# Optimization experiments

Hardware: AMD Instinct MI355X
Metric: run time of the kernel (lower is better)

## Reference

```python
import jax, jax.numpy as jnp
import numpy as np

BINS = 50
MIN_V = 0.0
MAX_V = 1.0
SIGMA = 10.0
DELTA = (MAX_V - MIN_V) / BINS
EPS = 1e-8


def _soft_bin(v, centers):
    # v: [N, D] -> [N, bins, D]
    d = v[:, None, :] - centers[None, :, None]
    return jax.nn.sigmoid(SIGMA * (d + DELTA / 2)) - jax.nn.sigmoid(SIGMA * (d - DELTA / 2))


def setup_inputs() -> dict:
    key = jax.random.key(0)
    k1, k2 = jax.random.split(key)
    im1 = jax.random.uniform(k1, (8, 384, 384), dtype=jnp.float32)
    im2 = jax.random.uniform(k2, (8, 384, 384), dtype=jnp.float32)
    return {"im1": im1, "im2": im2}


def reference(im1, im2):
    n = im1.shape[0]
    x = im1.reshape(n, -1)
    y = im2.reshape(n, -1)
    centers = MIN_V + DELTA * (jnp.arange(BINS, dtype=jnp.float32) + 0.5)
    xs = _soft_bin(x, centers)  # [N, bins, D]
    ys = _soft_bin(y, centers)  # [N, bins, D]
    hgram = jnp.einsum('nbd,ncd->nbc', xs, ys)  # [N, bins, bins]
    # NOTE: original normalizes by the sum over the WHOLE batch
    p_xy = hgram / jnp.sum(hgram)
    marginal_x = jnp.sum(p_xy, axis=2)  # [N, bins]
    marginal_y = jnp.sum(p_xy, axis=1)  # [N, bins]
    joined = marginal_x[:, :, None] * marginal_y[:, None, :]  # [N, bins, bins]
    mi_per = jnp.sum(
        p_xy * (jnp.log(p_xy + EPS) - jnp.log(joined + EPS)), axis=(1, 2)
    )
    return jnp.sum(mi_per)  # reduction='sum'
```

## Files before the change

### kernel.cpp

```cpp
#include <hip/hip_runtime.h>


#define D_TOTAL   147456
#define NBATCH    8
#define BINS      50
#define NEDGE     28
#define KSLICES   96
#define KC        256
#define SLICE_LEN (D_TOTAL / KSLICES)
#define ITERS     (SLICE_LEN / KC)
#define LDS_STR   280

typedef _Float16 half8  __attribute__((ext_vector_type(8)));
typedef __fp16   fp16x2 __attribute__((ext_vector_type(2)));
typedef float    f32x4  __attribute__((ext_vector_type(4)));

struct Tab { float c[NEDGE]; };
constexpr Tab make_tab() {
    Tab t{};
    double c = 0.6703200460356393;
    const double lam = 1.4918246976412703;
    for (int i = 0; i < NEDGE; ++i) { t.c[i] = (float)c; c *= lam; }
    return t;
}
constexpr Tab TAB = make_tab();

__global__ __launch_bounds__(256, 3) void hgram_kernel(const float* __restrict__ im1,
                                                       const float* __restrict__ im2,
                                                       float* __restrict__ hg) {
    __shared__ __align__(16) _Float16 Xs[32][LDS_STR];
    __shared__ __align__(16) _Float16 Ys[32][LDS_STR];

    const int tid   = threadIdx.x;
    const int slice = blockIdx.x;
    const int n     = blockIdx.y;
    const int base  = n * D_TOTAL + slice * SLICE_LEN;

    {
        unsigned* px = (unsigned*)&Xs[28][0];
        unsigned* py = (unsigned*)&Ys[28][0];
        for (int i = tid; i < 4 * LDS_STR / 2; i += 256) { px[i] = 0u; py[i] = 0u; }
    }

    const int h    = tid & 127;
    const int isY  = tid >> 7;
    const float2* src2 = (const float2*)((isY ? im2 : im1) + base);
    _Float16* plane = isY ? &Ys[0][0] : &Xs[0][0];
    _Float16* dst   = plane + 2 * h;

    const int lane = tid & 63;
    const int w    = tid >> 6;
    const int r0   = (w & 1) << 4;
    const int c0   = (w >> 1) << 4;
    const int frow = lane & 15;
    const int kg   = (lane >> 4) << 3;

    f32x4 acc = {0.f, 0.f, 0.f, 0.f};

    float2 v = src2[h];
    for (int it = 0; it < ITERS; ++it) {
        float2 nv = {0.f, 0.f};
        if (it + 1 < ITERS) nv = src2[(it + 1) * (KC / 2) + h];
        {
            const float Ea = __builtin_amdgcn_exp2f(v.x * -14.426950408889634f);
            const float Eb = __builtin_amdgcn_exp2f(v.y * -14.426950408889634f);
            #pragma unroll
            for (int i = 0; i < NEDGE; ++i) {
                const float c = TAB.c[i];
                float ta = __builtin_amdgcn_rcpf(__builtin_fmaf(c * Ea, 0.00390625f, 0.00390625f));
                float tb = __builtin_amdgcn_rcpf(__builtin_fmaf(c * Eb, 0.00390625f, 0.00390625f));
                fp16x2 p = __builtin_amdgcn_cvt_pkrtz(ta, tb);
                *(fp16x2*)(dst + i * LDS_STR) = p;
            }
        }
        __syncthreads();
        #pragma unroll
        for (int ks = 0; ks < 8; ++ks) {
            const int k0 = ks * 32 + kg;
            half8 a = *(const half8*)&Xs[r0 + frow][k0];
            half8 b = *(const half8*)&Ys[c0 + frow][k0];
            acc = __builtin_amdgcn_mfma_f32_16x16x32_f16(a, b, acc, 0, 0, 0);
        }
        __syncthreads();
        v = nv;
    }

    float* hgn = hg + n * 1024;
    const int gj = c0 + (lane & 15);
    const int ri = r0 + ((lane >> 4) << 2);
    if (gj < NEDGE) {
        #pragma unroll
        for (int r = 0; r < 4; ++r) {
            const int gi = ri + r;
            if (gi < NEDGE) atomicAdd(&hgn[gi * 32 + gj], acc[r]);
        }
    }
}

__global__ __launch_bounds__(1024) void finalize_kernel(const float* __restrict__ hg,
                                                        float* __restrict__ out) {
    __shared__ float Gs[NBATCH][NEDGE][29];
    __shared__ float mx[NBATCH][BINS], my[NBATCH][BINS];
    __shared__ float red[16];
    __shared__ float sT;
    const int tid = threadIdx.x;

    for (int idx = tid; idx < NBATCH * NEDGE * NEDGE; idx += 1024) {
        int n = idx / (NEDGE * NEDGE);
        int rem = idx - n * (NEDGE * NEDGE);
        int r = rem / NEDGE, c = rem - r * NEDGE;
        Gs[n][r][c] = hg[n * 1024 + r * 32 + c];
    }
    __syncthreads();

    if (tid < 2 * NBATCH * BINS) {
        const int which = (tid >= NBATCH * BINS) ? 1 : 0;
        const int t2 = which ? tid - NBATCH * BINS : tid;
        const int n = t2 / BINS, b = t2 - n * BINS;
        const int q = b >> 1;
        float w0, w1, w2, w3;
        if (b & 1) { w0 = -1.f; w1 = 9.f; w2 = -7.f; w3 = -1.f; }
        else       { w0 =  1.f; w1 = 7.f; w2 = -9.f; w3 =  1.f; }
        float m;
        if (which == 0) {
            m = w0 * (Gs[n][q][1]   - Gs[n][q][26])
              + w1 * (Gs[n][q+1][1] - Gs[n][q+1][26])
              + w2 * (Gs[n][q+2][1] - Gs[n][q+2][26])
              + w3 * (Gs[n][q+3][1] - Gs[n][q+3][26]);
            mx[n][b] = m * 0.0625f;
        } else {
            m = w0 * (Gs[n][1][q]   - Gs[n][26][q])
              + w1 * (Gs[n][1][q+1] - Gs[n][26][q+1])
              + w2 * (Gs[n][1][q+2] - Gs[n][26][q+2])
              + w3 * (Gs[n][1][q+3] - Gs[n][26][q+3]);
            my[n][b] = m * 0.0625f;
        }
    }
    if (tid == 0) {
        float t = 0.f;
        for (int n = 0; n < NBATCH; ++n)
            t += Gs[n][1][1] - Gs[n][1][26] - Gs[n][26][1] + Gs[n][26][26];
        sT = t;
    }
    __syncthreads();

    const float invT = 1.0f / sT;
    const float invT2 = invT * invT;
    float mi = 0.f;
    for (int task = tid; task < NBATCH * 25 * 25; task += 1024) {
        const int n = task / 625;
        const int rem = task - n * 625;
        const int bp = rem / 25, cp = rem - bp * 25;
        float g[4][4];
        #pragma unroll
        for (int r = 0; r < 4; ++r)
            #pragma unroll
            for (int s = 0; s < 4; ++s) g[r][s] = Gs[n][bp + r][cp + s];
        float rde[4], rdo[4];
        #pragma unroll
        for (int r = 0; r < 4; ++r) {
            rde[r] =  g[r][0] + 7.f * g[r][1] - 9.f * g[r][2] + g[r][3];
            rdo[r] = -g[r][0] + 9.f * g[r][1] - 7.f * g[r][2] - g[r][3];
        }
        const float hee = ( rde[0] + 7.f*rde[1] - 9.f*rde[2] + rde[3]) * (1.f/256.f);
        const float heo = ( rdo[0] + 7.f*rdo[1] - 9.f*rdo[2] + rdo[3]) * (1.f/256.f);
        const float hoe = (-rde[0] + 9.f*rde[1] - 7.f*rde[2] - rde[3]) * (1.f/256.f);
        const float hoo = (-rdo[0] + 9.f*rdo[1] - 7.f*rdo[2] - rdo[3]) * (1.f/256.f);
        const int b0 = 2 * bp, c0 = 2 * cp;
        {
            float p = hee * invT, jo = mx[n][b0] * my[n][c0] * invT2;
            mi += p * (__logf(p + 1e-8f) - __logf(jo + 1e-8f));
        }
        {
            float p = heo * invT, jo = mx[n][b0] * my[n][c0 + 1] * invT2;
            mi += p * (__logf(p + 1e-8f) - __logf(jo + 1e-8f));
        }
        {
            float p = hoe * invT, jo = mx[n][b0 + 1] * my[n][c0] * invT2;
            mi += p * (__logf(p + 1e-8f) - __logf(jo + 1e-8f));
        }
        {
            float p = hoo * invT, jo = mx[n][b0 + 1] * my[n][c0 + 1] * invT2;
            mi += p * (__logf(p + 1e-8f) - __logf(jo + 1e-8f));
        }
    }
    #pragma unroll
    for (int o = 32; o > 0; o >>= 1) mi += __shfl_down(mi, o, 64);
    if ((tid & 63) == 0) red[tid >> 6] = mi;
    __syncthreads();
    if (tid == 0) {
        float t = 0.f;
        for (int i = 0; i < 16; ++i) t += red[i];
        out[0] = t;
    }
}

extern "C" void kernel_launch(void* const* d_in, const int* in_sizes, int n_in,
                              void* d_out, int out_size, void* d_ws, size_t ws_size,
                              hipStream_t stream) {
    const float* im1 = (const float*)d_in[0];
    const float* im2 = (const float*)d_in[1];
    float* out = (float*)d_out;
    float* hg  = (float*)d_ws;

    (void)hipMemsetAsync(d_ws, 0, NBATCH * 1024 * sizeof(float), stream);
    hgram_kernel<<<dim3(KSLICES, NBATCH), dim3(256), 0, stream>>>(im1, im2, hg);
    finalize_kernel<<<dim3(1), dim3(1024), 0, stream>>>(hg, out);
}
```

Before: 83.01 us.

## Alternate staging between wave pairs and use 32x32 MFMA with K-split reduction

Each wave now converts four pixels per lane with float4 loads. Only one pair of waves (one X wave, one Y wave) stages each tile, alternating by iteration and prefetching two tiles ahead. The matrix product changes from four 16x16 output tiles to every wave computing the full 32x32 tile over its own quarter of K with the 32x32x16 MFMA. Partial tiles are then summed through LDS scratch before a single set of global atomics. The aim is to spread the sigmoid-table VALU work across iterations and cut redundant LDS reads and atomic traffic, at the cost of a longer per-iteration staging path on fewer waves.

```diff
diff --git a/kernel.cpp b/kernel.cpp
--- a/kernel.cpp
+++ b/kernel.cpp
@@ -14,6 +14,7 @@
 typedef _Float16 half8  __attribute__((ext_vector_type(8)));
 typedef __fp16   fp16x2 __attribute__((ext_vector_type(2)));
 typedef float    f32x4  __attribute__((ext_vector_type(4)));
+typedef float    f32x16 __attribute__((ext_vector_type(16)));
 
 struct Tab { float c[NEDGE]; };
 constexpr Tab make_tab() {
@@ -42,57 +43,75 @@
         for (int i = tid; i < 4 * LDS_STR / 2; i += 256) { px[i] = 0u; py[i] = 0u; }
     }
 
-    const int h    = tid & 127;
-    const int isY  = tid >> 7;
-    const float2* src2 = (const float2*)((isY ? im2 : im1) + base);
-    _Float16* plane = isY ? &Ys[0][0] : &Xs[0][0];
-    _Float16* dst   = plane + 2 * h;
-
     const int lane = tid & 63;
-    const int w    = tid >> 6;
-    const int r0   = (w & 1) << 4;
-    const int c0   = (w >> 1) << 4;
-    const int frow = lane & 15;
-    const int kg   = (lane >> 4) << 3;
-
-    f32x4 acc = {0.f, 0.f, 0.f, 0.f};
-
-    float2 v = src2[h];
+    const int sw   = tid >> 6;
+    const int pair = sw >> 1;
+    const int isY  = sw & 1;
+    const float4* src4 = (const float4*)((isY ? im2 : im1) + base);
+    _Float16* dst = (isY ? &Ys[0][0] : &Xs[0][0]) + 4 * lane;
+
+    auto stage = [&](float4 v) {
+        const float E0 = __builtin_amdgcn_exp2f(v.x * -14.426950408889634f);
+        const float E1 = __builtin_amdgcn_exp2f(v.y * -14.426950408889634f);
+        const float E2 = __builtin_amdgcn_exp2f(v.z * -14.426950408889634f);
+        const float E3 = __builtin_amdgcn_exp2f(v.w * -14.426950408889634f);
+        #pragma unroll
+        for (int i = 0; i < NEDGE; ++i) {
+            const float c = TAB.c[i];
+            float t0 = __builtin_amdgcn_rcpf(__builtin_fmaf(c * E0, 0.00390625f, 0.00390625f));
+            float t1 = __builtin_amdgcn_rcpf(__builtin_fmaf(c * E1, 0.00390625f, 0.00390625f));
+            float t2 = __builtin_amdgcn_rcpf(__builtin_fmaf(c * E2, 0.00390625f, 0.00390625f));
+            float t3 = __builtin_amdgcn_rcpf(__builtin_fmaf(c * E3, 0.00390625f, 0.00390625f));
+            uint2 U;
+            U.x = __builtin_bit_cast(unsigned, __builtin_amdgcn_cvt_pkrtz(t0, t1));
+            U.y = __builtin_bit_cast(unsigned, __builtin_amdgcn_cvt_pkrtz(t2, t3));
+            *(uint2*)(dst + i * LDS_STR) = U;
+        }
+    };
+
+    f32x16 acc = {0.f};
+    const int arow = lane & 31;
+    const int kgrp = (lane >> 5) << 3;
+
+    float4 v = src4[pair * (KC / 4) * 1 + lane + (pair ? (KC / 4) - (KC / 4) : 0)];
+    v = pair ? src4[(KC / 4) + lane] : src4[lane];
+
     for (int it = 0; it < ITERS; ++it) {
-        float2 nv = {0.f, 0.f};
-        if (it + 1 < ITERS) nv = src2[(it + 1) * (KC / 2) + h];
-        {
-            const float Ea = __builtin_amdgcn_exp2f(v.x * -14.426950408889634f);
-            const float Eb = __builtin_amdgcn_exp2f(v.y * -14.426950408889634f);
+        if ((it & 1) == pair) {
+            float4 nv = {0.f, 0.f, 0.f, 0.f};
+            if (it + 2 < ITERS) nv = src4[(it + 2) * (KC / 4) + lane];
+            stage(v);
+            v = nv;
+        }
+        __syncthreads();
+        #pragma unroll
+        for (int ks = 0; ks < 4; ++ks) {
+            const int k0 = sw * 64 + ks * 16 + kgrp;
+            half8 a = *(const half8*)&Xs[arow][k0];
+            half8 b = *(const half8*)&Ys[arow][k0];
+            acc = __builtin_amdgcn_mfma_f32_32x32x16_f16(a, b, acc, 0, 0, 0);
+        }
+        __syncthreads();
+    }
+
+    float* scratch = (float*)&Xs[0][0];
+    #pragma unroll
+    for (int r = 0; r < 16; ++r) {
+        const int row = (r & 3) + 8 * (r >> 2) + 4 * (lane >> 5);
+        scratch[sw * 1024 + row * 32 + (lane & 31)] = acc[r];
+    }
+    __syncthreads();
+    {
+        f32x4 s = *(const f32x4*)&scratch[4 * tid];
+        s += *(const f32x4*)&scratch[1024 + 4 * tid];
+        s += *(const f32x4*)&scratch[2048 + 4 * tid];
+        s += *(const f32x4*)&scratch[3072 + 4 * tid];
+        float* hgn = hg + n * 1024;
+        const int row = tid >> 3, col0 = (tid & 7) << 2;
+        if (row < NEDGE) {
             #pragma unroll
-            for (int i = 0; i < NEDGE; ++i) {
-                const float c = TAB.c[i];
-                float ta = __builtin_amdgcn_rcpf(__builtin_fmaf(c * Ea, 0.00390625f, 0.00390625f));
-                float tb = __builtin_amdgcn_rcpf(__builtin_fmaf(c * Eb, 0.00390625f, 0.00390625f));
-                fp16x2 p = __builtin_amdgcn_cvt_pkrtz(ta, tb);
-                *(fp16x2*)(dst + i * LDS_STR) = p;
-            }
-        }
-        __syncthreads();
-        #pragma unroll
-        for (int ks = 0; ks < 8; ++ks) {
-            const int k0 = ks * 32 + kg;
-            half8 a = *(const half8*)&Xs[r0 + frow][k0];
-            half8 b = *(const half8*)&Ys[c0 + frow][k0];
-            acc = __builtin_amdgcn_mfma_f32_16x16x32_f16(a, b, acc, 0, 0, 0);
-        }
-        __syncthreads();
-        v = nv;
-    }
-
-    float* hgn = hg + n * 1024;
-    const int gj = c0 + (lane & 15);
-    const int ri = r0 + ((lane >> 4) << 2);
-    if (gj < NEDGE) {
-        #pragma unroll
-        for (int r = 0; r < 4; ++r) {
-            const int gi = ri + r;
-            if (gi < NEDGE) atomicAdd(&hgn[gi * 32 + gj], acc[r]);
+            for (int j = 0; j < 4; ++j)
+                if (col0 + j < NEDGE) atomicAdd(&hgn[row * 32 + col0 + j], s[j]);
         }
     }
 }
```

Result: slower. 95.78 us (+15.4%).
